# Performance work log

Measured on AMD Instinct MI355X. Metric: run time of the kernel, lower is better.

Reference implementation:

```python
import jax, jax.numpy as jnp
import numpy as np

B, L, E = 256, 500, 300  # bsz, max_doc_len, word_embed_dim
KS = [3, 5, 7]           # filters_size


def setup_inputs() -> dict:
    key = jax.random.key(0)
    ks = jax.random.split(key, 1 + 2 * len(KS))
    inp = {"x": jax.random.normal(ks[0], (B, L, E), jnp.float32)}
    i = 1
    for k in KS:
        # PyTorch Conv2d default init scale ~ 1/sqrt(fan_in)
        inp[f"aw{k}"] = jax.random.normal(ks[i], (k, E), jnp.float32) / np.sqrt(k * E).astype(np.float32); i += 1
        inp[f"ab{k}"] = jnp.zeros((1,), jnp.float32)
        inp[f"cw{k}"] = jax.random.normal(ks[i], (E,), jnp.float32) / np.sqrt(E).astype(np.float32); i += 1
        inp[f"cb{k}"] = jnpp = jnp.zeros((1,), jnp.float32)
    return inp


def _branch(x, aw, ab, cw, cb):
    # x: (B, L, E); aw: (k, E); cw: (E,)
    k = aw.shape[0]
    p = (k - 1) // 2
    x4 = x[:, None, :, :]            # NCHW: (B, 1, L, E)
    w4 = aw[None, None, :, :]        # OIHW: (1, 1, k, E)
    s = jax.lax.conv_general_dilated(x4, w4, window_strides=(1, 1),
                                     padding=((p, p), (0, 0)))  # (B, 1, L, 1)
    score = jax.nn.sigmoid(s + ab[0])[:, 0, :, :]               # (B, L, 1)
    gated = x * score                                           # broadcast over E
    # Conv2d(1,1,(1,E)) == per-timestep dot product over E
    return jnp.tanh(jnp.einsum('ble,e->bl', gated, cw) + cb[0])  # (B, L)


def reference(x, aw3, ab3, cw3, cb3, aw5, ab5, cw5, cb5, aw7, ab7, cw7, cb7):
    return (_branch(x, aw3, ab3, cw3, cb3),
            _branch(x, aw5, ab5, cw5, cb5),
            _branch(x, aw7, ab7, cw7, cb7))
```

## Files before the change

kernel.cpp:

```cpp
#include <hip/hip_runtime.h>
#include <math.h>

#define BB 256
#define LL 500
#define EE 300
#define NROWS (BB * LL)
#define NJ 18

__global__ __launch_bounds__(256) void dots_kernel(
    const float* __restrict__ x,
    const float* __restrict__ aw3, const float* __restrict__ cw3,
    const float* __restrict__ aw5, const float* __restrict__ cw5,
    const float* __restrict__ aw7, const float* __restrict__ cw7,
    float* __restrict__ dots)
{
    const int tid  = blockIdx.x * blockDim.x + threadIdx.x;
    const int wave = tid >> 6;
    const int lane = threadIdx.x & 63;
    const int g    = lane >> 4;
    const int j    = lane & 15;
    const int r0   = wave * 16 + g * 4;

    const float4* __restrict__ xr0 = (const float4*)(x + (size_t)(r0 + 0) * EE);
    const float4* __restrict__ xr1 = (const float4*)(x + (size_t)(r0 + 1) * EE);
    const float4* __restrict__ xr2 = (const float4*)(x + (size_t)(r0 + 2) * EE);
    const float4* __restrict__ xr3 = (const float4*)(x + (size_t)(r0 + 3) * EE);

    const float* const wptr[NJ] = {
        aw3, aw3 + 300, aw3 + 600, cw3,
        aw5, aw5 + 300, aw5 + 600, aw5 + 900, aw5 + 1200, cw5,
        aw7, aw7 + 300, aw7 + 600, aw7 + 900, aw7 + 1200, aw7 + 1500, aw7 + 1800, cw7
    };

    float acc[NJ][4];
#pragma unroll
    for (int d = 0; d < NJ; ++d)
#pragma unroll
        for (int rr = 0; rr < 4; ++rr) acc[d][rr] = 0.0f;

#define BODY(c)                                                                     \
    {                                                                               \
        const float4 x0 = xr0[(c)];                                                 \
        const float4 x1 = xr1[(c)];                                                 \
        const float4 x2 = xr2[(c)];                                                 \
        const float4 x3 = xr3[(c)];                                                 \
        _Pragma("unroll")                                                           \
        for (int d = 0; d < NJ; ++d) {                                              \
            const float4 w = ((const float4*)wptr[d])[(c)];                         \
            acc[d][0] = fmaf(x0.w, w.w, fmaf(x0.z, w.z, fmaf(x0.y, w.y, fmaf(x0.x, w.x, acc[d][0])))); \
            acc[d][1] = fmaf(x1.w, w.w, fmaf(x1.z, w.z, fmaf(x1.y, w.y, fmaf(x1.x, w.x, acc[d][1])))); \
            acc[d][2] = fmaf(x2.w, w.w, fmaf(x2.z, w.z, fmaf(x2.y, w.y, fmaf(x2.x, w.x, acc[d][2])))); \
            acc[d][3] = fmaf(x3.w, w.w, fmaf(x3.z, w.z, fmaf(x3.y, w.y, fmaf(x3.x, w.x, acc[d][3])))); \
        }                                                                           \
    }

    BODY(j)
    BODY(j + 16)
    BODY(j + 32)
    BODY(j + 48)
    if (j < 11) {
        BODY(j + 64)
    }
#undef BODY

#pragma unroll
    for (int d = 0; d < NJ; ++d)
#pragma unroll
        for (int rr = 0; rr < 4; ++rr) {
            float v = acc[d][rr];
            v += __shfl_xor(v, 1, 16);
            v += __shfl_xor(v, 2, 16);
            v += __shfl_xor(v, 4, 16);
            v += __shfl_xor(v, 8, 16);
            acc[d][rr] = v;
        }

#pragma unroll
    for (int rr = 0; rr < 4; ++rr) {
        if (j == rr) {
            const int r = r0 + rr;
#pragma unroll
            for (int d = 0; d < NJ; ++d) dots[(size_t)d * NROWS + r] = acc[d][rr];
        }
    }
}

__global__ __launch_bounds__(256) void combine_kernel(
    const float* __restrict__ dots,
    const float* __restrict__ ab3, const float* __restrict__ cb3,
    const float* __restrict__ ab5, const float* __restrict__ cb5,
    const float* __restrict__ ab7, const float* __restrict__ cb7,
    float* __restrict__ out)
{
    const int r = blockIdx.x * blockDim.x + threadIdx.x;
    if (r >= NROWS) return;
    const int l = r % LL;

    float pre3 = 0.0f, pre5 = 0.0f, pre7 = 0.0f;

#pragma unroll
    for (int t = 0; t < 3; ++t) {
        const int lo = l + t - 1;
        if (lo >= 0 && lo < LL) pre3 += dots[(size_t)t * NROWS + (r + t - 1)];
    }
#pragma unroll
    for (int t = 0; t < 5; ++t) {
        const int lo = l + t - 2;
        if (lo >= 0 && lo < LL) pre5 += dots[(size_t)(4 + t) * NROWS + (r + t - 2)];
    }
#pragma unroll
    for (int t = 0; t < 7; ++t) {
        const int lo = l + t - 3;
        if (lo >= 0 && lo < LL) pre7 += dots[(size_t)(10 + t) * NROWS + (r + t - 3)];
    }

    const float c3v = dots[(size_t)3 * NROWS + r];
    const float c5v = dots[(size_t)9 * NROWS + r];
    const float c7v = dots[(size_t)17 * NROWS + r];

    const float s3 = 1.0f / (1.0f + expf(-(pre3 + ab3[0])));
    const float s5 = 1.0f / (1.0f + expf(-(pre5 + ab5[0])));
    const float s7 = 1.0f / (1.0f + expf(-(pre7 + ab7[0])));

    out[r]              = tanhf(s3 * c3v + cb3[0]);
    out[NROWS + r]      = tanhf(s5 * c5v + cb5[0]);
    out[2 * NROWS + r]  = tanhf(s7 * c7v + cb7[0]);
}

extern "C" void kernel_launch(void* const* d_in, const int* in_sizes, int n_in,
                              void* d_out, int out_size, void* d_ws, size_t ws_size,
                              hipStream_t stream) {
    const float* x   = (const float*)d_in[0];
    const float* aw3 = (const float*)d_in[1];
    const float* ab3 = (const float*)d_in[2];
    const float* cw3 = (const float*)d_in[3];
    const float* cb3 = (const float*)d_in[4];
    const float* aw5 = (const float*)d_in[5];
    const float* ab5 = (const float*)d_in[6];
    const float* cw5 = (const float*)d_in[7];
    const float* cb5 = (const float*)d_in[8];
    const float* aw7 = (const float*)d_in[9];
    const float* ab7 = (const float*)d_in[10];
    const float* cw7 = (const float*)d_in[11];
    const float* cb7 = (const float*)d_in[12];

    float* dots = (float*)d_ws;
    float* out  = (float*)d_out;

    dots_kernel<<<2000, 256, 0, stream>>>(x, aw3, cw3, aw5, cw5, aw7, cw7, dots);

    const int blocks = (NROWS + 255) / 256;
    combine_kernel<<<blocks, 256, 0, stream>>>(dots, ab3, cb3, ab5, cb5, ab7, cb7, out);
}
```

Before: 259.7 us.

## Fuse dot-product and combine kernels with halo-tiled shared memory stage

Merges the two kernels into one: each block handles one batch row's 56-position tile plus a 3-row halo on each side, keeping the 18 per-row dot products in shared memory instead of a global workspace. The sigmoid/tanh combine then reads neighbours from LDS, with out-of-range rows zeroed to act as padding. This removes the intermediate global write/read and one launch, at the cost of recomputing halo rows (about 14% extra dot work) and a mostly idle combine phase.

New measurement: 266.4 us. 2.6% more time.

```diff
diff --git a/kernel.cpp b/kernel.cpp
--- a/kernel.cpp
+++ b/kernel.cpp
@@ -6,25 +6,40 @@
 #define EE 300
 #define NROWS (BB * LL)
 #define NJ 18
+#define TOUT 56
+#define NTILE 9
+#define DROWS 64
 
-__global__ __launch_bounds__(256) void dots_kernel(
+__global__ __launch_bounds__(256) void fused_kernel(
     const float* __restrict__ x,
-    const float* __restrict__ aw3, const float* __restrict__ cw3,
-    const float* __restrict__ aw5, const float* __restrict__ cw5,
-    const float* __restrict__ aw7, const float* __restrict__ cw7,
-    float* __restrict__ dots)
+    const float* __restrict__ aw3, const float* __restrict__ ab3,
+    const float* __restrict__ cw3, const float* __restrict__ cb3,
+    const float* __restrict__ aw5, const float* __restrict__ ab5,
+    const float* __restrict__ cw5, const float* __restrict__ cb5,
+    const float* __restrict__ aw7, const float* __restrict__ ab7,
+    const float* __restrict__ cw7, const float* __restrict__ cb7,
+    float* __restrict__ out)
 {
-    const int tid  = blockIdx.x * blockDim.x + threadIdx.x;
-    const int wave = tid >> 6;
+    __shared__ float dlds[DROWS][NJ + 1];
+
+    const int b    = blockIdx.x / NTILE;
+    const int t    = blockIdx.x % NTILE;
+    const int l0   = t * TOUT - 3;
+    const int wave = threadIdx.x >> 6;
     const int lane = threadIdx.x & 63;
     const int g    = lane >> 4;
     const int j    = lane & 15;
-    const int r0   = wave * 16 + g * 4;
+    const int lr   = wave * 16 + g * 4;
 
-    const float4* __restrict__ xr0 = (const float4*)(x + (size_t)(r0 + 0) * EE);
-    const float4* __restrict__ xr1 = (const float4*)(x + (size_t)(r0 + 1) * EE);
-    const float4* __restrict__ xr2 = (const float4*)(x + (size_t)(r0 + 2) * EE);
-    const float4* __restrict__ xr3 = (const float4*)(x + (size_t)(r0 + 3) * EE);
+    bool valid[4];
+    const float4* xr[4];
+#pragma unroll
+    for (int rr = 0; rr < 4; ++rr) {
+        const int l = l0 + lr + rr;
+        valid[rr] = (l >= 0) && (l < LL);
+        const int lc = l < 0 ? 0 : (l >= LL ? LL - 1 : l);
+        xr[rr] = (const float4*)(x + ((size_t)b * LL + lc) * EE);
+    }
 
     const float* const wptr[NJ] = {
         aw3, aw3 + 300, aw3 + 600, cw3,
@@ -40,10 +55,10 @@
 
 #define BODY(c)                                                                     \
     {                                                                               \
-        const float4 x0 = xr0[(c)];                                                 \
-        const float4 x1 = xr1[(c)];                                                 \
-        const float4 x2 = xr2[(c)];                                                 \
-        const float4 x3 = xr3[(c)];                                                 \
+        const float4 x0 = xr[0][(c)];                                               \
+        const float4 x1 = xr[1][(c)];                                               \
+        const float4 x2 = xr[2][(c)];                                               \
+        const float4 x3 = xr[3][(c)];                                               \
         _Pragma("unroll")                                                           \
         for (int d = 0; d < NJ; ++d) {                                              \
             const float4 w = ((const float4*)wptr[d])[(c)];                         \
@@ -78,53 +93,42 @@
 #pragma unroll
     for (int rr = 0; rr < 4; ++rr) {
         if (j == rr) {
-            const int r = r0 + rr;
+            const float vf = valid[rr] ? 1.0f : 0.0f;
 #pragma unroll
-            for (int d = 0; d < NJ; ++d) dots[(size_t)d * NROWS + r] = acc[d][rr];
+            for (int d = 0; d < NJ; ++d) dlds[lr + rr][d] = acc[d][rr] * vf;
         }
     }
-}
 
-__global__ __launch_bounds__(256) void combine_kernel(
-    const float* __restrict__ dots,
-    const float* __restrict__ ab3, const float* __restrict__ cb3,
-    const float* __restrict__ ab5, const float* __restrict__ cb5,
-    const float* __restrict__ ab7, const float* __restrict__ cb7,
-    float* __restrict__ out)
-{
-    const int r = blockIdx.x * blockDim.x + threadIdx.x;
-    if (r >= NROWS) return;
-    const int l = r % LL;
+    __syncthreads();
 
-    float pre3 = 0.0f, pre5 = 0.0f, pre7 = 0.0f;
+    const int tid = threadIdx.x;
+    if (tid < TOUT) {
+        const int lo = t * TOUT + tid;
+        if (lo < LL) {
+            const int c = tid + 3;
 
+            float pre3 = 0.0f, pre5 = 0.0f, pre7 = 0.0f;
 #pragma unroll
-    for (int t = 0; t < 3; ++t) {
-        const int lo = l + t - 1;
-        if (lo >= 0 && lo < LL) pre3 += dots[(size_t)t * NROWS + (r + t - 1)];
+            for (int tp = 0; tp < 3; ++tp) pre3 += dlds[c + tp - 1][tp];
+#pragma unroll
+            for (int tp = 0; tp < 5; ++tp) pre5 += dlds[c + tp - 2][4 + tp];
+#pragma unroll
+            for (int tp = 0; tp < 7; ++tp) pre7 += dlds[c + tp - 3][10 + tp];
+
+            const float c3v = dlds[c][3];
+            const float c5v = dlds[c][9];
+            const float c7v = dlds[c][17];
+
+            const float s3 = 1.0f / (1.0f + expf(-(pre3 + ab3[0])));
+            const float s5 = 1.0f / (1.0f + expf(-(pre5 + ab5[0])));
+            const float s7 = 1.0f / (1.0f + expf(-(pre7 + ab7[0])));
+
+            const int r = b * LL + lo;
+            out[r]             = tanhf(s3 * c3v + cb3[0]);
+            out[NROWS + r]     = tanhf(s5 * c5v + cb5[0]);
+            out[2 * NROWS + r] = tanhf(s7 * c7v + cb7[0]);
+        }
     }
-#pragma unroll
-    for (int t = 0; t < 5; ++t) {
-        const int lo = l + t - 2;
-        if (lo >= 0 && lo < LL) pre5 += dots[(size_t)(4 + t) * NROWS + (r + t - 2)];
-    }
-#pragma unroll
-    for (int t = 0; t < 7; ++t) {
-        const int lo = l + t - 3;
-        if (lo >= 0 && lo < LL) pre7 += dots[(size_t)(10 + t) * NROWS + (r + t - 3)];
-    }
-
-    const float c3v = dots[(size_t)3 * NROWS + r];
-    const float c5v = dots[(size_t)9 * NROWS + r];
-    const float c7v = dots[(size_t)17 * NROWS + r];
-
-    const float s3 = 1.0f / (1.0f + expf(-(pre3 + ab3[0])));
-    const float s5 = 1.0f / (1.0f + expf(-(pre5 + ab5[0])));
-    const float s7 = 1.0f / (1.0f + expf(-(pre7 + ab7[0])));
-
-    out[r]              = tanhf(s3 * c3v + cb3[0]);
-    out[NROWS + r]      = tanhf(s5 * c5v + cb5[0]);
-    out[2 * NROWS + r]  = tanhf(s7 * c7v + cb7[0]);
 }
 
 extern "C" void kernel_launch(void* const* d_in, const int* in_sizes, int n_in,
@@ -144,11 +148,8 @@
     const float* cw7 = (const float*)d_in[11];
     const float* cb7 = (const float*)d_in[12];
 
-    float* dots = (float*)d_ws;
-    float* out  = (float*)d_out;
+    float* out = (float*)d_out;
 
-    dots_kernel<<<2000, 256, 0, stream>>>(x, aw3, cw3, aw5, cw5, aw7, cw7, dots);
-
-    const int blocks = (NROWS + 255) / 256;
-    combine_kernel<<<blocks, 256, 0, stream>>>(dots, ab3, cb3, ab5, cb5, ab7, cb7, out);
+    fused_kernel<<<BB * NTILE, 256, 0, stream>>>(
+        x, aw3, ab3, cw3, cb3, aw5, ab5, cw5, cb5, aw7, ab7, cw7, cb7, out);
 }
```
